# Kernel tuning notes

Measured on AMD Instinct MI355X. Metric: run time of the kernel, lower is better.

## Reference

```python
import jax, jax.numpy as jnp
import numpy as np

TAU = 0.8
N, D = 4096, 512

def _proj(x, W, b):
    # nn.Linear then ELU (torch Linear: x @ W.T + b)
    return jax.nn.elu(x @ W.T + b)

def setup_inputs() -> dict:
    key = jax.random.key(0)
    k1, k2, k3, k4, k5 = jax.random.split(key, 5)
    v1 = jax.random.normal(k1, (N, D), dtype=jnp.float32)
    v2 = jax.random.normal(k2, (N, D), dtype=jnp.float32)
    pos = jax.random.uniform(k3, (N, N), dtype=jnp.float32)
    neg = jax.random.uniform(k4, (N, N), dtype=jnp.float32)
    W = jax.random.normal(k5, (D, D), dtype=jnp.float32) * (1.414 / np.sqrt(D))
    b = jnp.zeros((D,), dtype=jnp.float32)
    return {"v1_embs": v1, "v2_embs": v2, "pos": pos, "neg": neg, "W_proj": W, "b_proj": b}

def reference(v1_embs, v2_embs, pos, neg, W_proj, b_proj):
    z1 = _proj(v1_embs, W_proj, b_proj)
    z2 = _proj(v2_embs, W_proj, b_proj)
    # cosine-similarity style: dot / (|z1||z2|) / tau, then exp
    n1 = jnp.linalg.norm(z1, axis=-1, keepdims=True)  # [N,1]
    n2 = jnp.linalg.norm(z2, axis=-1, keepdims=True)  # [N,1]
    dots = z1 @ z2.T                                   # [N,N]
    sim = jnp.exp(dots / (n1 * n2.T) / TAU)
    sim_pos = sim * pos
    sim_neg = sim * neg
    ratio = sim_pos.sum() / (sim_pos + sim_neg).sum()
    return -jnp.log(ratio)
```

## Files before the change

### kernel.cpp

```cpp
#include <hip/hip_runtime.h>
#include <hip/hip_bf16.h>
#include <math.h>

#define NROWS 4096
#define DDIM  512
#define INV_TAU 1.25f
#define SROW 132

typedef __attribute__((ext_vector_type(8))) short short8;
typedef __attribute__((ext_vector_type(4))) float f32x4;

__device__ inline void gload_lds16(const void* g, void* l) {
  __builtin_amdgcn_global_load_lds(
      (const __attribute__((address_space(1))) void*)g,
      (__attribute__((address_space(3))) void*)l, 16, 0, 0);
}

__device__ inline unsigned short f2bf(float f) {
  __hip_bfloat16 h = __float2bfloat16(f);
  return __builtin_bit_cast(unsigned short, h);
}
__device__ inline float bf2f(unsigned short u) {
  return __bfloat162float(__builtin_bit_cast(__hip_bfloat16, u));
}

__global__ void convert_kernel(const float* __restrict__ v1,
                               const float* __restrict__ v2,
                               const float* __restrict__ W,
                               unsigned short* __restrict__ v1b,
                               unsigned short* __restrict__ v2b,
                               unsigned short* __restrict__ Wb,
                               float* __restrict__ nsq1,
                               float* __restrict__ nsq2) {
  int idx = blockIdx.x * blockDim.x + threadIdx.x;
  if (idx < NROWS) { nsq1[idx] = 0.f; nsq2[idx] = 0.f; }
  const int TOTV = (NROWS * DDIM) / 4;
  const int TOTW = (DDIM * DDIM) / 4;
  const int total = 2 * TOTV + TOTW;
  const int stride = gridDim.x * blockDim.x;
  for (int i = idx; i < total; i += stride) {
    const float4* src; unsigned short* dst; int j;
    if (i < TOTV)            { src = (const float4*)v1; dst = v1b; j = i; }
    else if (i < 2 * TOTV)   { src = (const float4*)v2; dst = v2b; j = i - TOTV; }
    else                     { src = (const float4*)W;  dst = Wb;  j = i - 2 * TOTV; }
    float4 x = src[j];
    ushort4 o;
    o.x = f2bf(x.x); o.y = f2bf(x.y); o.z = f2bf(x.z); o.w = f2bf(x.w);
    *(ushort4*)&dst[j * 4] = o;
  }
}

__global__ __launch_bounds__(256) void proj_kernel(
    const unsigned short* __restrict__ v1b, const unsigned short* __restrict__ v2b,
    const unsigned short* __restrict__ Wb,  const float* __restrict__ bias,
    unsigned short* __restrict__ z1b, unsigned short* __restrict__ z2b,
    float* __restrict__ nsq1, float* __restrict__ nsq2) {
  __shared__ __align__(16) unsigned short As[128 * 32];
  __shared__ __align__(16) unsigned short Bs[128 * 32];
  const int tid = threadIdx.x;
  const int wid = tid >> 6, lane = tid & 63;
  const int wm = wid >> 1, wn = wid & 1;
  const int l15 = lane & 15, l4 = lane >> 4;

  const int zsel = blockIdx.z;
  const unsigned short* Ag = (zsel ? v2b : v1b) + (size_t)blockIdx.y * 128 * DDIM;
  const unsigned short* Bg = Wb + (size_t)blockIdx.x * 128 * DDIM;
  unsigned short* Z = (zsel ? z2b : z1b);
  float* nsq = (zsel ? nsq2 : nsq1);

  f32x4 acc[4][4];
#pragma unroll
  for (int m = 0; m < 4; ++m)
#pragma unroll
    for (int n = 0; n < 4; ++n) acc[m][n] = (f32x4){0.f, 0.f, 0.f, 0.f};

  for (int kt = 0; kt < DDIM; kt += 32) {
#pragma unroll
    for (int i = 0; i < 2; ++i) {
      int off = i * 4096 + tid * 16;
      int row = off >> 6;
      int kb  = off & 63;
      gload_lds16((const char*)(Ag + row * DDIM + kt) + kb,
                  (char*)As + i * 4096 + wid * 1024);
      gload_lds16((const char*)(Bg + row * DDIM + kt) + kb,
                  (char*)Bs + i * 4096 + wid * 1024);
    }
    asm volatile("s_waitcnt vmcnt(0)" ::: "memory");
    __syncthreads();
    short8 av[4], bv[4];
#pragma unroll
    for (int m = 0; m < 4; ++m)
      av[m] = *(const short8*)&As[(wm * 64 + m * 16 + l15) * 32 + l4 * 8];
#pragma unroll
    for (int n = 0; n < 4; ++n)
      bv[n] = *(const short8*)&Bs[(wn * 64 + n * 16 + l15) * 32 + l4 * 8];
#pragma unroll
    for (int m = 0; m < 4; ++m)
#pragma unroll
      for (int n = 0; n < 4; ++n)
        acc[m][n] = __builtin_amdgcn_mfma_f32_16x16x32_bf16(
            av[m], bv[n], acc[m][n], 0, 0, 0);
    __syncthreads();
  }

  const int rowBase = blockIdx.y * 128 + wm * 64;
  const int colBase = blockIdx.x * 128 + wn * 64;
  float bcol[4];
#pragma unroll
  for (int n = 0; n < 4; ++n) bcol[n] = bias[colBase + n * 16 + l15];
#pragma unroll
  for (int m = 0; m < 4; ++m) {
#pragma unroll
    for (int reg = 0; reg < 4; ++reg) {
      int gRow = rowBase + m * 16 + l4 * 4 + reg;
      float rs = 0.f;
#pragma unroll
      for (int n = 0; n < 4; ++n) {
        int gCol = colBase + n * 16 + l15;
        float y = acc[m][n][reg] + bcol[n];
        float zv = (y > 0.f) ? y : expm1f(y);
        unsigned short zb = f2bf(zv);
        Z[(size_t)gRow * DDIM + gCol] = zb;
        float zf = bf2f(zb);
        rs += zf * zf;
      }
      rs += __shfl_xor(rs, 1, 64);
      rs += __shfl_xor(rs, 2, 64);
      rs += __shfl_xor(rs, 4, 64);
      rs += __shfl_xor(rs, 8, 64);
      if (l15 == 0) atomicAdd(&nsq[gRow], rs);
    }
  }
}

__global__ __launch_bounds__(256) void dots_kernel(
    const unsigned short* __restrict__ z1b, const unsigned short* __restrict__ z2b,
    const float* __restrict__ nsq1, const float* __restrict__ nsq2,
    const float* __restrict__ pos, const float* __restrict__ neg,
    double* __restrict__ partials) {
  __shared__ __align__(16) char smem[2][16384];
  float* sCh = (float*)smem;

  const int tid = threadIdx.x;
  const int wid = tid >> 6, lane = tid & 63;
  const int wm = wid >> 1, wn = wid & 1;
  const int l15 = lane & 15, l4 = lane >> 4;

  const int bid = blockIdx.x;
  const int swz = (bid & 7) * 128 + (bid >> 3);
  const int by = swz >> 5, bx = swz & 31;

  const unsigned short* Ag = z1b + (size_t)by * 128 * DDIM;
  const unsigned short* Bg = z2b + (size_t)bx * 128 * DDIM;

  f32x4 acc[4][4];
#pragma unroll
  for (int m = 0; m < 4; ++m)
#pragma unroll
    for (int n = 0; n < 4; ++n) acc[m][n] = (f32x4){0.f, 0.f, 0.f, 0.f};

#define STAGE(buf, kt)                                                         \
  {                                                                            \
    _Pragma("unroll")                                                          \
    for (int i = 0; i < 2; ++i) {                                              \
      int off = i * 4096 + tid * 16;                                           \
      int row = off >> 6;                                                      \
      int kb  = off & 63;                                                      \
      gload_lds16((const char*)(Ag + row * DDIM + (kt)) + kb,                  \
                  smem[buf] + i * 4096 + wid * 1024);                          \
      gload_lds16((const char*)(Bg + row * DDIM + (kt)) + kb,                  \
                  smem[buf] + 8192 + i * 4096 + wid * 1024);                   \
    }                                                                          \
  }

  STAGE(0, 0);
  asm volatile("s_waitcnt vmcnt(0)" ::: "memory");
  __syncthreads();

#pragma unroll
  for (int t = 0; t < 16; ++t) {
    const int cur = t & 1;
    if (t < 15) STAGE(cur ^ 1, (t + 1) * 32);
    const unsigned short* As = (const unsigned short*)smem[cur];
    const unsigned short* Bs = (const unsigned short*)(smem[cur] + 8192);
    short8 av[4], bv[4];
#pragma unroll
    for (int m = 0; m < 4; ++m)
      av[m] = *(const short8*)&As[(wm * 64 + m * 16 + l15) * 32 + l4 * 8];
#pragma unroll
    for (int n = 0; n < 4; ++n)
      bv[n] = *(const short8*)&Bs[(wn * 64 + n * 16 + l15) * 32 + l4 * 8];
#pragma unroll
    for (int m = 0; m < 4; ++m)
#pragma unroll
      for (int n = 0; n < 4; ++n)
        acc[m][n] = __builtin_amdgcn_mfma_f32_16x16x32_bf16(
            av[m], bv[n], acc[m][n], 0, 0, 0);
    asm volatile("s_waitcnt vmcnt(0)" ::: "memory");
    __syncthreads();
  }
#undef STAGE

  const int blockRow = by * 128;
  const int blockCol = bx * 128;
  const int rowBase = blockRow + wm * 64;
  const int colBase = blockCol + wn * 64;

  const int lr = tid >> 3;
  const int lcBase = (tid & 7) * 16;
  const int gRowRbase = blockRow + (lr >> 4) * 64 + (lr & 15);
  const int lrW = wm * 16 + l4 * 4;
  const int lcW = wn * 64 + l15;

  float4 pv[2][4], gv[2][4];
  {
    const float* pr = pos + (size_t)gRowRbase * NROWS + blockCol + lcBase;
    const float* gr = neg + (size_t)gRowRbase * NROWS + blockCol + lcBase;
#pragma unroll
    for (int i = 0; i < 4; ++i) {
      pv[0][i] = *(const float4*)(pr + 4 * i);
      gv[0][i] = *(const float4*)(gr + 4 * i);
    }
  }

  float rs2[4], rs1[4][4];
#pragma unroll
  for (int n = 0; n < 4; ++n) rs2[n] = rsqrtf(nsq2[colBase + n * 16 + l15]);
#pragma unroll
  for (int m = 0; m < 4; ++m)
#pragma unroll
    for (int reg = 0; reg < 4; ++reg)
      rs1[m][reg] = rsqrtf(nsq1[rowBase + m * 16 + l4 * 4 + reg]);

  float sumP = 0.f, sumT = 0.f;
#pragma unroll
  for (int m = 0; m < 4; ++m) {
    const int c = m & 1, o = c ^ 1;
#pragma unroll
    for (int reg = 0; reg < 4; ++reg) {
#pragma unroll
      for (int n = 0; n < 4; ++n) {
        float s = __expf(acc[m][n][reg] * (rs1[m][reg] * rs2[n]) * INV_TAU);
        sCh[(lrW + reg) * SROW + lcW + n * 16] = s;
      }
    }
    if (m < 3) {
      const float* pr = pos + (size_t)(gRowRbase + (m + 1) * 16) * NROWS + blockCol + lcBase;
      const float* gr = neg + (size_t)(gRowRbase + (m + 1) * 16) * NROWS + blockCol + lcBase;
#pragma unroll
      for (int i = 0; i < 4; ++i) {
        pv[o][i] = *(const float4*)(pr + 4 * i);
        gv[o][i] = *(const float4*)(gr + 4 * i);
      }
    }
    __syncthreads();
#pragma unroll
    for (int i = 0; i < 4; ++i) {
      float4 s4 = *(const float4*)&sCh[lr * SROW + lcBase + 4 * i];
      sumP += s4.x * pv[c][i].x + s4.y * pv[c][i].y + s4.z * pv[c][i].z + s4.w * pv[c][i].w;
      sumT += s4.x * (pv[c][i].x + gv[c][i].x) + s4.y * (pv[c][i].y + gv[c][i].y) +
              s4.z * (pv[c][i].z + gv[c][i].z) + s4.w * (pv[c][i].w + gv[c][i].w);
    }
    __syncthreads();
  }

#pragma unroll
  for (int sft = 1; sft < 64; sft <<= 1) {
    sumP += __shfl_xor(sumP, sft, 64);
    sumT += __shfl_xor(sumT, sft, 64);
  }
  __shared__ float redP[4], redT[4];
  if (lane == 0) { redP[wid] = sumP; redT[wid] = sumT; }
  __syncthreads();
  if (tid == 0) {
    double tp = (double)redP[0] + redP[1] + redP[2] + redP[3];
    double tt = (double)redT[0] + redT[1] + redT[2] + redT[3];
    partials[2 * bid]     = tp;
    partials[2 * bid + 1] = tt;
  }
}

__global__ void finalize_kernel(const double* __restrict__ partials,
                                float* __restrict__ out) {
  __shared__ double sp[256], st[256];
  int t = threadIdx.x;
  double a = 0.0, b = 0.0;
  for (int i = t; i < 1024; i += 256) {
    a += partials[2 * i];
    b += partials[2 * i + 1];
  }
  sp[t] = a; st[t] = b;
  __syncthreads();
  for (int s = 128; s > 0; s >>= 1) {
    if (t < s) { sp[t] += sp[t + s]; st[t] += st[t + s]; }
    __syncthreads();
  }
  if (t == 0) out[0] = (float)(log(st[0]) - log(sp[0]));
}

extern "C" void kernel_launch(void* const* d_in, const int* in_sizes, int n_in,
                              void* d_out, int out_size, void* d_ws, size_t ws_size,
                              hipStream_t stream) {
  (void)in_sizes; (void)n_in; (void)out_size; (void)ws_size;
  const float* v1   = (const float*)d_in[0];
  const float* v2   = (const float*)d_in[1];
  const float* pos  = (const float*)d_in[2];
  const float* neg  = (const float*)d_in[3];
  const float* W    = (const float*)d_in[4];
  const float* bias = (const float*)d_in[5];

  char* ws = (char*)d_ws;
  unsigned short* z1b = (unsigned short*)(ws + 0);
  unsigned short* z2b = (unsigned short*)(ws + 4194304);
  unsigned short* v1b = (unsigned short*)(ws + 8388608);
  unsigned short* v2b = (unsigned short*)(ws + 12582912);
  unsigned short* Wb  = (unsigned short*)(ws + 16777216);
  float* nsq1         = (float*)(ws + 17301504);
  float* nsq2         = (float*)(ws + 17317888);
  double* partials    = (double*)(ws + 17334272);
  float* out = (float*)d_out;

  hipLaunchKernelGGL(convert_kernel, dim3(1024), dim3(256), 0, stream,
                     v1, v2, W, v1b, v2b, Wb, nsq1, nsq2);
  hipLaunchKernelGGL(proj_kernel, dim3(DDIM / 128, NROWS / 128, 2), dim3(256), 0, stream,
                     v1b, v2b, Wb, bias, z1b, z2b, nsq1, nsq2);
  hipLaunchKernelGGL(dots_kernel, dim3(1024), dim3(256), 0, stream,
                     z1b, z2b, nsq1, nsq2, pos, neg, partials);
  hipLaunchKernelGGL(finalize_kernel, dim3(1), dim3(256), 0, stream,
                     partials, out);
}
```

Before: 85.71 us.

## Restructure dots kernel pipeline with two-ahead prefetch, setprio, and lower register pressure

The dots kernel now targets 4 waves per SIMD via launch bounds and stops prefetching pos/neg and holding all rs1 values, which cuts register use. The K loop issues loads two stages ahead, waits with vmcnt(4) instead of fully draining, uses raw s_barrier, and raises wave priority around the MFMA block. The block-index swizzle is dropped in favour of plain row-major tile order, which may lower L2 reuse of z1/z2 tiles. Loading pos/neg without double-buffering exposes their memory latency in the epilogue, which the higher occupancy is meant to hide.

```diff
diff --git a/kernel.cpp b/kernel.cpp
--- a/kernel.cpp
+++ b/kernel.cpp
@@ -133,7 +133,7 @@
   }
 }
 
-__global__ __launch_bounds__(256) void dots_kernel(
+__global__ __launch_bounds__(256, 4) void dots_kernel(
     const unsigned short* __restrict__ z1b, const unsigned short* __restrict__ z2b,
     const float* __restrict__ nsq1, const float* __restrict__ nsq2,
     const float* __restrict__ pos, const float* __restrict__ neg,
@@ -147,8 +147,7 @@
   const int l15 = lane & 15, l4 = lane >> 4;
 
   const int bid = blockIdx.x;
-  const int swz = (bid & 7) * 128 + (bid >> 3);
-  const int by = swz >> 5, bx = swz & 31;
+  const int by = bid >> 5, bx = bid & 31;
 
   const unsigned short* Ag = z1b + (size_t)by * 128 * DDIM;
   const unsigned short* Bg = z2b + (size_t)bx * 128 * DDIM;
@@ -159,30 +158,30 @@
 #pragma unroll
     for (int n = 0; n < 4; ++n) acc[m][n] = (f32x4){0.f, 0.f, 0.f, 0.f};
 
-#define STAGE(buf, kt)                                                         \
+#define STAGE(buf, t)                                                          \
   {                                                                            \
     _Pragma("unroll")                                                          \
     for (int i = 0; i < 2; ++i) {                                              \
       int off = i * 4096 + tid * 16;                                           \
       int row = off >> 6;                                                      \
       int kb  = off & 63;                                                      \
-      gload_lds16((const char*)(Ag + row * DDIM + (kt)) + kb,                  \
+      gload_lds16((const char*)Ag + row * 1024 + (t) * 64 + kb,                \
                   smem[buf] + i * 4096 + wid * 1024);                          \
-      gload_lds16((const char*)(Bg + row * DDIM + (kt)) + kb,                  \
+      gload_lds16((const char*)Bg + row * 1024 + (t) * 64 + kb,                \
                   smem[buf] + 8192 + i * 4096 + wid * 1024);                   \
     }                                                                          \
   }
 
   STAGE(0, 0);
-  asm volatile("s_waitcnt vmcnt(0)" ::: "memory");
-  __syncthreads();
+  STAGE(1, 1);
 
 #pragma unroll
   for (int t = 0; t < 16; ++t) {
-    const int cur = t & 1;
-    if (t < 15) STAGE(cur ^ 1, (t + 1) * 32);
-    const unsigned short* As = (const unsigned short*)smem[cur];
-    const unsigned short* Bs = (const unsigned short*)(smem[cur] + 8192);
+    if (t < 15) asm volatile("s_waitcnt vmcnt(4)" ::: "memory");
+    else        asm volatile("s_waitcnt vmcnt(0)" ::: "memory");
+    __builtin_amdgcn_s_barrier();
+    const unsigned short* As = (const unsigned short*)smem[t & 1];
+    const unsigned short* Bs = (const unsigned short*)(smem[t & 1] + 8192);
     short8 av[4], bv[4];
 #pragma unroll
     for (int m = 0; m < 4; ++m)
@@ -190,14 +189,16 @@
 #pragma unroll
     for (int n = 0; n < 4; ++n)
       bv[n] = *(const short8*)&Bs[(wn * 64 + n * 16 + l15) * 32 + l4 * 8];
+    __builtin_amdgcn_s_setprio(1);
 #pragma unroll
     for (int m = 0; m < 4; ++m)
 #pragma unroll
       for (int n = 0; n < 4; ++n)
         acc[m][n] = __builtin_amdgcn_mfma_f32_16x16x32_bf16(
             av[m], bv[n], acc[m][n], 0, 0, 0);
-    asm volatile("s_waitcnt vmcnt(0)" ::: "memory");
-    __syncthreads();
+    __builtin_amdgcn_s_setprio(0);
+    __builtin_amdgcn_s_barrier();
+    if (t < 14) STAGE(t & 1, t + 2);
   }
 #undef STAGE
 
@@ -205,6 +206,10 @@
   const int blockCol = bx * 128;
   const int rowBase = blockRow + wm * 64;
   const int colBase = blockCol + wn * 64;
+
+  float rs2[4];
+#pragma unroll
+  for (int n = 0; n < 4; ++n) rs2[n] = rsqrtf(nsq2[colBase + n * 16 + l15]);
 
   const int lr = tid >> 3;
   const int lcBase = (tid & 7) * 16;
@@ -212,54 +217,33 @@
   const int lrW = wm * 16 + l4 * 4;
   const int lcW = wn * 64 + l15;
 
-  float4 pv[2][4], gv[2][4];
-  {
-    const float* pr = pos + (size_t)gRowRbase * NROWS + blockCol + lcBase;
-    const float* gr = neg + (size_t)gRowRbase * NROWS + blockCol + lcBase;
+  float sumP = 0.f, sumT = 0.f;
+#pragma unroll
+  for (int m = 0; m < 4; ++m) {
+    const float* pr = pos + (size_t)(gRowRbase + m * 16) * NROWS + blockCol + lcBase;
+    const float* gr = neg + (size_t)(gRowRbase + m * 16) * NROWS + blockCol + lcBase;
+    float4 pv[4], gv[4];
 #pragma unroll
     for (int i = 0; i < 4; ++i) {
-      pv[0][i] = *(const float4*)(pr + 4 * i);
-      gv[0][i] = *(const float4*)(gr + 4 * i);
-    }
-  }
-
-  float rs2[4], rs1[4][4];
-#pragma unroll
-  for (int n = 0; n < 4; ++n) rs2[n] = rsqrtf(nsq2[colBase + n * 16 + l15]);
-#pragma unroll
-  for (int m = 0; m < 4; ++m)
-#pragma unroll
-    for (int reg = 0; reg < 4; ++reg)
-      rs1[m][reg] = rsqrtf(nsq1[rowBase + m * 16 + l4 * 4 + reg]);
-
-  float sumP = 0.f, sumT = 0.f;
-#pragma unroll
-  for (int m = 0; m < 4; ++m) {
-    const int c = m & 1, o = c ^ 1;
+      pv[i] = *(const float4*)(pr + 4 * i);
+      gv[i] = *(const float4*)(gr + 4 * i);
+    }
 #pragma unroll
     for (int reg = 0; reg < 4; ++reg) {
+      float rs1 = rsqrtf(nsq1[rowBase + m * 16 + l4 * 4 + reg]);
 #pragma unroll
       for (int n = 0; n < 4; ++n) {
-        float s = __expf(acc[m][n][reg] * (rs1[m][reg] * rs2[n]) * INV_TAU);
+        float s = __expf(acc[m][n][reg] * (rs1 * rs2[n]) * INV_TAU);
         sCh[(lrW + reg) * SROW + lcW + n * 16] = s;
       }
     }
-    if (m < 3) {
-      const float* pr = pos + (size_t)(gRowRbase + (m + 1) * 16) * NROWS + blockCol + lcBase;
-      const float* gr = neg + (size_t)(gRowRbase + (m + 1) * 16) * NROWS + blockCol + lcBase;
-#pragma unroll
-      for (int i = 0; i < 4; ++i) {
-        pv[o][i] = *(const float4*)(pr + 4 * i);
-        gv[o][i] = *(const float4*)(gr + 4 * i);
-      }
-    }
     __syncthreads();
 #pragma unroll
     for (int i = 0; i < 4; ++i) {
       float4 s4 = *(const float4*)&sCh[lr * SROW + lcBase + 4 * i];
-      sumP += s4.x * pv[c][i].x + s4.y * pv[c][i].y + s4.z * pv[c][i].z + s4.w * pv[c][i].w;
-      sumT += s4.x * (pv[c][i].x + gv[c][i].x) + s4.y * (pv[c][i].y + gv[c][i].y) +
-              s4.z * (pv[c][i].z + gv[c][i].z) + s4.w * (pv[c][i].w + gv[c][i].w);
+      sumP += s4.x * pv[i].x + s4.y * pv[i].y + s4.z * pv[i].z + s4.w * pv[i].w;
+      sumT += s4.x * (pv[i].x + gv[i].x) + s4.y * (pv[i].y + gv[i].y) +
+              s4.z * (pv[i].z + gv[i].z) + s4.w * (pv[i].w + gv[i].w);
     }
     __syncthreads();
   }
```

Result: faster. 75.27 us (-12.2%).
